# Kernel tuning notes

Measured on AMD Instinct MI355X. Metric: run time of the kernel, lower is better.

Reference implementation:

```python
import jax, jax.numpy as jnp
import numpy as np

N_NODES = 100000
N_EDGES = 1600000
N_GRAPHS = 512
IN_DIM = 128
HID = 128


def setup_inputs() -> dict:
    key = jax.random.key(0)
    ks = jax.random.split(key, 8)
    x = jax.random.normal(ks[0], (N_NODES, IN_DIM), dtype=jnp.float32)
    edge_index = jax.random.randint(ks[1], (2, N_EDGES), 0, N_NODES, dtype=jnp.int64)
    batch = jnp.sort(jax.random.randint(ks[2], (N_NODES,), 0, N_GRAPHS, dtype=jnp.int64))
    s1 = 1.0 / np.sqrt(IN_DIM)
    s2 = 1.0 / np.sqrt(HID)
    W1 = jax.random.normal(ks[3], (IN_DIM, HID), dtype=jnp.float32) * s1
    b1 = jnp.zeros((HID,), dtype=jnp.float32)
    W2 = jax.random.normal(ks[4], (HID, HID), dtype=jnp.float32) * s2
    b2 = jnp.zeros((HID,), dtype=jnp.float32)
    Wp = jax.random.normal(ks[5], (HID, 1), dtype=jnp.float32) * s2
    bp = jnp.zeros((1,), dtype=jnp.float32)
    return {"x": x, "edge_index": edge_index, "batch": batch,
            "W1": W1, "b1": b1, "W2": W2, "b2": b2, "Wp": Wp, "bp": bp}


def _gcn_conv(x, W, b, src, dst, deg_inv_sqrt):
    # PyG GCNConv: linear transform, then normalized scatter-add (self-loops
    # already appended to src/dst), then bias.
    h = x @ W                                   # [N, H]
    norm = deg_inv_sqrt[src] * deg_inv_sqrt[dst]  # [E+N]
    msg = h[src] * norm[:, None]                # gather + scale
    out = jax.ops.segment_sum(msg, dst, num_segments=N_NODES)
    return out + b


def reference(x, edge_index, batch, W1, b1, W2, b2, Wp, bp):
    # Add self-loops once; degree (with self-loops) over target nodes.
    si = jnp.arange(N_NODES, dtype=edge_index.dtype)
    src = jnp.concatenate([edge_index[0], si])
    dst = jnp.concatenate([edge_index[1], si])
    ones = jnp.ones(src.shape[0], dtype=x.dtype)
    deg = jax.ops.segment_sum(ones, dst, num_segments=N_NODES)
    deg_inv_sqrt = jnp.where(deg > 0, jax.lax.rsqrt(jnp.maximum(deg, 1.0)), 0.0)

    h = jax.nn.relu(_gcn_conv(x, W1, b1, src, dst, deg_inv_sqrt))  # dropout = identity (eval)
    h = jax.nn.relu(_gcn_conv(h, W2, b2, src, dst, deg_inv_sqrt))

    # global_mean_pool over graph ids
    sums = jax.ops.segment_sum(h, batch, num_segments=N_GRAPHS)
    cnts = jax.ops.segment_sum(jnp.ones(N_NODES, dtype=h.dtype), batch, num_segments=N_GRAPHS)
    pooled = sums / jnp.maximum(cnts, 1.0)[:, None]               # [G, H]

    return (pooled @ Wp + bp).squeeze(-1)                          # [G]
```

## Files before the change

kernel.cpp:

```cpp
#include <hip/hip_runtime.h>
#include <hip/hip_bf16.h>

#define NN 100000
#define NG 512
#define H  128

typedef _Float16 half8 __attribute__((ext_vector_type(8)));
typedef float f32x4 __attribute__((ext_vector_type(4)));

__global__ __launch_bounds__(256) void k_hist(const int* __restrict__ dst,
                                              int* __restrict__ deg, int E) {
    int e = blockIdx.x * 256 + threadIdx.x;
    if (e < E) atomicAdd(&deg[dst[e]], 1);
}

__global__ __launch_bounds__(256) void k_scan_block(const int* __restrict__ deg,
                                                    int* __restrict__ rowptr,
                                                    int* __restrict__ bsum, int n) {
    __shared__ int s[256];
    int tid = threadIdx.x;
    int i = blockIdx.x * 256 + tid;
    int v = (i < n) ? deg[i] : 0;
    s[tid] = v;
    __syncthreads();
    #pragma unroll
    for (int off = 1; off < 256; off <<= 1) {
        int t = (tid >= off) ? s[tid - off] : 0;
        __syncthreads();
        s[tid] += t;
        __syncthreads();
    }
    if (i < n) rowptr[i] = s[tid] - v;
    if (tid == 255) bsum[blockIdx.x] = s[255];
}

__global__ __launch_bounds__(512) void k_scan_top(int* __restrict__ bsum, int nb) {
    __shared__ int s[512];
    int tid = threadIdx.x;
    int v = (tid < nb) ? bsum[tid] : 0;
    s[tid] = v;
    __syncthreads();
    #pragma unroll
    for (int off = 1; off < 512; off <<= 1) {
        int t = (tid >= off) ? s[tid - off] : 0;
        __syncthreads();
        s[tid] += t;
        __syncthreads();
    }
    if (tid < nb) bsum[tid] = s[tid] - v;
}

__global__ __launch_bounds__(256) void k_scan_fin(int* __restrict__ rowptr,
                                                  const int* __restrict__ bsum,
                                                  const int* __restrict__ deg,
                                                  int* __restrict__ cursor,
                                                  float* __restrict__ dinv,
                                                  int n, int E) {
    int i = blockIdx.x * 256 + threadIdx.x;
    if (i >= n) return;
    int r = rowptr[i] + bsum[i >> 8];
    rowptr[i] = r;
    cursor[i] = r;
    dinv[i] = rsqrtf((float)deg[i] + 1.0f);
    if (i == 0) rowptr[n] = E;
}

__global__ __launch_bounds__(256) void k_wprep(const float* __restrict__ W1,
                                               const float* __restrict__ W2,
                                               _Float16* __restrict__ Wt1,
                                               _Float16* __restrict__ Wt2) {
    int bb = blockIdx.x;
    const float* W = (bb < 64) ? W1 : W2;
    _Float16* Wt = (bb < 64) ? Wt1 : Wt2;
    int i = (bb & 63) * 256 + threadIdx.x;
    int k = i >> 7, n = i & 127;
    Wt[n * 128 + k] = (_Float16)W[i];
}

__global__ __launch_bounds__(256) void k_fill_gemm1(
        const int* __restrict__ src, const int* __restrict__ dst,
        int* __restrict__ cursor, int* __restrict__ col, int E, int nfb,
        const float* __restrict__ x, const _Float16* __restrict__ Wt1,
        const float* __restrict__ dinv, _Float16* __restrict__ tS, int n) {
    if ((int)blockIdx.x < nfb) {
        int e = blockIdx.x * 256 + threadIdx.x;
        if (e >= E) return;
        int d = dst[e];
        int pos = atomicAdd(&cursor[d], 1);
        col[pos] = src[e];
        return;
    }
    const int row0 = ((int)blockIdx.x - nfb) * 64;
    const int tid = threadIdx.x;
    const int w = tid >> 6, lane = tid & 63;
    const int l16 = lane & 15, quad = lane >> 4;
    const int Arow = row0 + w * 16 + l16;
    f32x4 acc[8] = {};
    #pragma unroll
    for (int kk = 0; kk < 4; ++kk) {
        half8 af;
        if (Arow < n) {
            const float* ap = x + (size_t)Arow * H + kk * 32 + quad * 8;
            float4 a0 = ((const float4*)ap)[0];
            float4 a1 = ((const float4*)ap)[1];
            af[0] = (_Float16)a0.x; af[1] = (_Float16)a0.y;
            af[2] = (_Float16)a0.z; af[3] = (_Float16)a0.w;
            af[4] = (_Float16)a1.x; af[5] = (_Float16)a1.y;
            af[6] = (_Float16)a1.z; af[7] = (_Float16)a1.w;
        } else {
            #pragma unroll
            for (int j = 0; j < 8; ++j) af[j] = (_Float16)0.0f;
        }
        #pragma unroll
        for (int nt = 0; nt < 8; ++nt) {
            half8 bf = *((const half8*)(Wt1 + (nt * 16 + l16) * H + kk * 32 + quad * 8));
            acc[nt] = __builtin_amdgcn_mfma_f32_16x16x32_f16(af, bf, acc[nt], 0, 0, 0);
        }
    }
    #pragma unroll
    for (int r = 0; r < 4; ++r) {
        int R = row0 + w * 16 + quad * 4 + r;
        if (R < n) {
            float sc = dinv[R];
            _Float16* crow = tS + (size_t)R * H + l16;
            #pragma unroll
            for (int nt = 0; nt < 8; ++nt)
                crow[nt * 16] = (_Float16)(acc[nt][r] * sc);
        }
    }
}

__global__ __launch_bounds__(256) void k_gemm2(const _Float16* __restrict__ h1,
                                               const _Float16* __restrict__ Wt2,
                                               const float* __restrict__ dinv,
                                               _Float16* __restrict__ tS2, int n) {
    const int row0 = blockIdx.x * 64;
    const int tid = threadIdx.x;
    const int w = tid >> 6, lane = tid & 63;
    const int l16 = lane & 15, quad = lane >> 4;
    const int Arow = row0 + w * 16 + l16;
    f32x4 acc[8] = {};
    #pragma unroll
    for (int kk = 0; kk < 4; ++kk) {
        half8 af;
        if (Arow < n) {
            af = ((const half8*)(h1 + (size_t)Arow * H))[kk * 4 + quad];
        } else {
            #pragma unroll
            for (int j = 0; j < 8; ++j) af[j] = (_Float16)0.0f;
        }
        #pragma unroll
        for (int nt = 0; nt < 8; ++nt) {
            half8 bf = *((const half8*)(Wt2 + (nt * 16 + l16) * H + kk * 32 + quad * 8));
            acc[nt] = __builtin_amdgcn_mfma_f32_16x16x32_f16(af, bf, acc[nt], 0, 0, 0);
        }
    }
    #pragma unroll
    for (int r = 0; r < 4; ++r) {
        int R = row0 + w * 16 + quad * 4 + r;
        if (R < n) {
            float sc = dinv[R];
            _Float16* crow = tS2 + (size_t)R * H + l16;
            #pragma unroll
            for (int nt = 0; nt < 8; ++nt)
                crow[nt * 16] = (_Float16)(acc[nt][r] * sc);
        }
    }
}

__device__ __forceinline__ void gather_rows_h(const half8* __restrict__ t8,
                                              const int* __restrict__ col,
                                              int node, int e0, int end,
                                              float acc[8]) {
    const int lane = threadIdx.x & 63;
    const int q = lane >> 4;
    const int l16 = lane & 15;
    float a0[8] = {}, a1[8] = {};
    if (q == 0) {
        half8 v = t8[(size_t)node * 16 + l16];
        #pragma unroll
        for (int i = 0; i < 8; ++i) a0[i] = (float)v[i];
    }
    for (int base = e0; base < end; base += 64) {
        int ce = base + lane;
        int cidx = (ce < end) ? col[ce] : 0;
        int m = min(64, end - base);
        int nf = m >> 2;
        int g = 0;
        for (; g + 2 <= nf; g += 2) {
            int s0 = __shfl(cidx, 4 * g + q);
            int s1 = __shfl(cidx, 4 * g + 4 + q);
            half8 v0 = t8[(size_t)s0 * 16 + l16];
            half8 v1 = t8[(size_t)s1 * 16 + l16];
            #pragma unroll
            for (int i = 0; i < 8; ++i) {
                a0[i] += (float)v0[i];
                a1[i] += (float)v1[i];
            }
        }
        if (g < nf) {
            int s0 = __shfl(cidx, 4 * g + q);
            half8 v0 = t8[(size_t)s0 * 16 + l16];
            #pragma unroll
            for (int i = 0; i < 8; ++i) a0[i] += (float)v0[i];
        }
        int tail = m & 3;
        if (tail) {
            int s = __shfl(cidx, 4 * nf + q);
            if (q < tail) {
                half8 v = t8[(size_t)s * 16 + l16];
                #pragma unroll
                for (int i = 0; i < 8; ++i) a0[i] += (float)v[i];
            }
        }
    }
    #pragma unroll
    for (int i = 0; i < 8; ++i) {
        float t = a0[i] + a1[i];
        t += __shfl_xor(t, 16);
        t += __shfl_xor(t, 32);
        acc[i] = t;
    }
}

__global__ __launch_bounds__(256) void k_gather1(const _Float16* __restrict__ tS,
                                                 const int* __restrict__ rowptr,
                                                 const int* __restrict__ col,
                                                 const float* __restrict__ dinv,
                                                 const float* __restrict__ b,
                                                 _Float16* __restrict__ out, int n) {
    int node = blockIdx.x * 4 + (threadIdx.x >> 6);
    int lane = threadIdx.x & 63;
    int q = lane >> 4, l16 = lane & 15;
    if (node >= n) return;
    int e0 = rowptr[node], end = rowptr[node + 1];
    float acc[8];
    gather_rows_h((const half8*)tS, col, node, e0, end, acc);
    if (q == 0) {
        float dn = dinv[node];
        const float4* b4 = (const float4*)b;
        float4 bb0 = b4[2 * l16], bb1 = b4[2 * l16 + 1];
        half8 hv;
        hv[0] = (_Float16)fmaxf(dn * acc[0] + bb0.x, 0.0f);
        hv[1] = (_Float16)fmaxf(dn * acc[1] + bb0.y, 0.0f);
        hv[2] = (_Float16)fmaxf(dn * acc[2] + bb0.z, 0.0f);
        hv[3] = (_Float16)fmaxf(dn * acc[3] + bb0.w, 0.0f);
        hv[4] = (_Float16)fmaxf(dn * acc[4] + bb1.x, 0.0f);
        hv[5] = (_Float16)fmaxf(dn * acc[5] + bb1.y, 0.0f);
        hv[6] = (_Float16)fmaxf(dn * acc[6] + bb1.z, 0.0f);
        hv[7] = (_Float16)fmaxf(dn * acc[7] + bb1.w, 0.0f);
        ((half8*)out)[(size_t)node * 16 + l16] = hv;
    }
}

__global__ __launch_bounds__(256) void k_gather2(const _Float16* __restrict__ tS,
                                                 const int* __restrict__ rowptr,
                                                 const int* __restrict__ col,
                                                 const float* __restrict__ dinv,
                                                 const float* __restrict__ b,
                                                 const float* __restrict__ Wp,
                                                 const int* __restrict__ batch,
                                                 float* __restrict__ pool,
                                                 float* __restrict__ cnt, int n) {
    int node = blockIdx.x * 4 + (threadIdx.x >> 6);
    int lane = threadIdx.x & 63;
    int l16 = lane & 15;
    if (node >= n) return;
    int e0 = rowptr[node], end = rowptr[node + 1];
    float acc[8];
    gather_rows_h((const half8*)tS, col, node, e0, end, acc);
    float dn = dinv[node];
    const float4* b4 = (const float4*)b;
    const float4* w4 = (const float4*)Wp;
    float4 bb0 = b4[2 * l16], bb1 = b4[2 * l16 + 1];
    float4 wp0 = w4[2 * l16], wp1 = w4[2 * l16 + 1];
    float s = fmaxf(dn * acc[0] + bb0.x, 0.0f) * wp0.x +
              fmaxf(dn * acc[1] + bb0.y, 0.0f) * wp0.y +
              fmaxf(dn * acc[2] + bb0.z, 0.0f) * wp0.z +
              fmaxf(dn * acc[3] + bb0.w, 0.0f) * wp0.w +
              fmaxf(dn * acc[4] + bb1.x, 0.0f) * wp1.x +
              fmaxf(dn * acc[5] + bb1.y, 0.0f) * wp1.y +
              fmaxf(dn * acc[6] + bb1.z, 0.0f) * wp1.z +
              fmaxf(dn * acc[7] + bb1.w, 0.0f) * wp1.w;
    s += __shfl_xor(s, 1);
    s += __shfl_xor(s, 2);
    s += __shfl_xor(s, 4);
    s += __shfl_xor(s, 8);
    if (lane == 0) {
        int g = batch[node];
        atomicAdd(&pool[g], s);
        atomicAdd(&cnt[g], 1.0f);
    }
}

__global__ __launch_bounds__(256) void final_out_kernel(const float* __restrict__ pool,
                                                        const float* __restrict__ cnt,
                                                        const float* __restrict__ bp,
                                                        float* __restrict__ out, int g) {
    int i = blockIdx.x * 256 + threadIdx.x;
    if (i < g) out[i] = pool[i] / fmaxf(cnt[i], 1.0f) + bp[0];
}

extern "C" void kernel_launch(void* const* d_in, const int* in_sizes, int n_in,
                              void* d_out, int out_size, void* d_ws, size_t ws_size,
                              hipStream_t stream) {
    const float* x     = (const float*)d_in[0];
    const int*   ei    = (const int*)d_in[1];
    const int*   batch = (const int*)d_in[2];
    const float* W1    = (const float*)d_in[3];
    const float* b1    = (const float*)d_in[4];
    const float* W2    = (const float*)d_in[5];
    const float* b2    = (const float*)d_in[6];
    const float* Wp    = (const float*)d_in[7];
    const float* bp    = (const float*)d_in[8];
    float* out = (float*)d_out;

    const int E = in_sizes[1] / 2;
    const int* src = ei;
    const int* dst = ei + E;

    const size_t BUFH = (size_t)NN * H * sizeof(_Float16);
    const size_t NI   = 401408;
    char* ws = (char*)d_ws;
    size_t off = 0;
    _Float16* tS   = (_Float16*)(ws + off); off += BUFH;
    _Float16* h1   = (_Float16*)(ws + off); off += BUFH;
    _Float16* tS2  = (_Float16*)(ws + off); off += BUFH;
    int*      deg  = (int*)     (ws + off); off += NI;
    int*   rowptr  = (int*)     (ws + off); off += NI;
    int*   cursor  = (int*)     (ws + off); off += NI;
    float*    dinv = (float*)   (ws + off); off += NI;
    int*      col  = (int*)     (ws + off); off += ((size_t)E * 4 + 4095) / 4096 * 4096;
    _Float16* Wt1  = (_Float16*)(ws + off); off += 32768;
    _Float16* Wt2  = (_Float16*)(ws + off); off += 32768;
    int*      bsum = (int*)     (ws + off); off += 4096;
    float*    pool = (float*)   (ws + off); off += 2048;
    float*    cnt  = (float*)   (ws + off); off += 2048;

    const int NB  = (NN + 255) / 256;
    const int NFB = (E + 255) / 256;
    const int NGB = (NN + 63) / 64;

    hipMemsetAsync(deg, 0, NN * sizeof(int), stream);
    hipMemsetAsync(pool, 0, 4096, stream);
    k_wprep<<<128, 256, 0, stream>>>(W1, W2, Wt1, Wt2);
    k_hist<<<NFB, 256, 0, stream>>>(dst, deg, E);
    k_scan_block<<<NB, 256, 0, stream>>>(deg, rowptr, bsum, NN);
    k_scan_top<<<1, 512, 0, stream>>>(bsum, NB);
    k_scan_fin<<<NB, 256, 0, stream>>>(rowptr, bsum, deg, cursor, dinv, NN, E);

    k_fill_gemm1<<<NFB + NGB, 256, 0, stream>>>(src, dst, cursor, col, E, NFB,
                                                x, Wt1, dinv, tS, NN);

    k_gather1<<<(NN + 3) / 4, 256, 0, stream>>>(tS, rowptr, col, dinv, b1, h1, NN);
    k_gemm2<<<NGB, 256, 0, stream>>>(h1, Wt2, dinv, tS2, NN);

    k_gather2<<<(NN + 3) / 4, 256, 0, stream>>>(tS2, rowptr, col, dinv, b2, Wp,
                                                batch, pool, cnt, NN);

    final_out_kernel<<<(NG + 255) / 256, 256, 0, stream>>>(pool, cnt, bp, out, NG);
}
```

Before: 688.0 us.

## Split neighbor gathers into feature slices across blocks for cache locality

Replaces the one-wavefront-per-node gather with a feature-sliced scheme. Each block handles one 16-feature slice (32 bytes per row) for 32 nodes, with 8 lanes per node reading half2 values. The intent is to shrink the working set of each gather pass so random row accesses hit in L2/MALL more often, and to raise parallelism per node. The cost is narrower 4-byte loads, repeated reads of the col index for each slice, and pooling partials spread over 8 atomic slots per graph that a final reduction has to sum.

```diff
diff --git a/kernel.cpp b/kernel.cpp
--- a/kernel.cpp
+++ b/kernel.cpp
@@ -6,6 +6,7 @@
 #define H  128
 
 typedef _Float16 half8 __attribute__((ext_vector_type(8)));
+typedef _Float16 half2v __attribute__((ext_vector_type(2)));
 typedef float f32x4 __attribute__((ext_vector_type(4)));
 
 __global__ __launch_bounds__(256) void k_hist(const int* __restrict__ dst,
@@ -168,137 +169,98 @@
     }
 }
 
-__device__ __forceinline__ void gather_rows_h(const half8* __restrict__ t8,
-                                              const int* __restrict__ col,
-                                              int node, int e0, int end,
-                                              float acc[8]) {
+__device__ __forceinline__ float2 gather_slice(const _Float16* __restrict__ tS,
+                                               const int* __restrict__ col,
+                                               int node, int e0, int end, int foff) {
     const int lane = threadIdx.x & 63;
-    const int q = lane >> 4;
-    const int l16 = lane & 15;
-    float a0[8] = {}, a1[8] = {};
-    if (q == 0) {
-        half8 v = t8[(size_t)node * 16 + l16];
+    const int li = lane & 7;
+    const int gb = lane & 56;
+    float ax, ay, bx = 0.f, by = 0.f;
+    {
+        half2v v = *((const half2v*)(tS + (size_t)node * H + foff));
+        ax = (float)v[0]; ay = (float)v[1];
+    }
+    for (int c = e0; c < end; c += 8) {
+        int ce = c + li;
+        int cidx = (ce < end) ? col[ce] : 0;
+        int m = end - c;
         #pragma unroll
-        for (int i = 0; i < 8; ++i) a0[i] = (float)v[i];
-    }
-    for (int base = e0; base < end; base += 64) {
-        int ce = base + lane;
-        int cidx = (ce < end) ? col[ce] : 0;
-        int m = min(64, end - base);
-        int nf = m >> 2;
-        int g = 0;
-        for (; g + 2 <= nf; g += 2) {
-            int s0 = __shfl(cidx, 4 * g + q);
-            int s1 = __shfl(cidx, 4 * g + 4 + q);
-            half8 v0 = t8[(size_t)s0 * 16 + l16];
-            half8 v1 = t8[(size_t)s1 * 16 + l16];
-            #pragma unroll
-            for (int i = 0; i < 8; ++i) {
-                a0[i] += (float)v0[i];
-                a1[i] += (float)v1[i];
-            }
-        }
-        if (g < nf) {
-            int s0 = __shfl(cidx, 4 * g + q);
-            half8 v0 = t8[(size_t)s0 * 16 + l16];
-            #pragma unroll
-            for (int i = 0; i < 8; ++i) a0[i] += (float)v0[i];
-        }
-        int tail = m & 3;
-        if (tail) {
-            int s = __shfl(cidx, 4 * nf + q);
-            if (q < tail) {
-                half8 v = t8[(size_t)s * 16 + l16];
-                #pragma unroll
-                for (int i = 0; i < 8; ++i) a0[i] += (float)v[i];
-            }
-        }
-    }
-    #pragma unroll
-    for (int i = 0; i < 8; ++i) {
-        float t = a0[i] + a1[i];
-        t += __shfl_xor(t, 16);
-        t += __shfl_xor(t, 32);
-        acc[i] = t;
-    }
-}
-
-__global__ __launch_bounds__(256) void k_gather1(const _Float16* __restrict__ tS,
-                                                 const int* __restrict__ rowptr,
-                                                 const int* __restrict__ col,
-                                                 const float* __restrict__ dinv,
-                                                 const float* __restrict__ b,
-                                                 _Float16* __restrict__ out, int n) {
-    int node = blockIdx.x * 4 + (threadIdx.x >> 6);
-    int lane = threadIdx.x & 63;
-    int q = lane >> 4, l16 = lane & 15;
+        for (int j = 0; j < 8; j += 2) {
+            int s0 = __shfl(cidx, gb + j);
+            int s1 = __shfl(cidx, gb + j + 1);
+            half2v v0 = *((const half2v*)(tS + (size_t)s0 * H + foff));
+            half2v v1 = *((const half2v*)(tS + (size_t)s1 * H + foff));
+            bool ok0 = (j < m), ok1 = (j + 1 < m);
+            ax += ok0 ? (float)v0[0] : 0.0f;
+            ay += ok0 ? (float)v0[1] : 0.0f;
+            bx += ok1 ? (float)v1[0] : 0.0f;
+            by += ok1 ? (float)v1[1] : 0.0f;
+        }
+    }
+    return make_float2(ax + bx, ay + by);
+}
+
+__global__ __launch_bounds__(256) void k_gather1s(const _Float16* __restrict__ tS,
+                                                  const int* __restrict__ rowptr,
+                                                  const int* __restrict__ col,
+                                                  const float* __restrict__ dinv,
+                                                  const float* __restrict__ b,
+                                                  _Float16* __restrict__ out, int n) {
+    int f = blockIdx.x & 7;
+    int node = (blockIdx.x >> 3) * 32 + (threadIdx.x >> 3);
     if (node >= n) return;
+    int li = threadIdx.x & 7;
+    int foff = f * 16 + li * 2;
     int e0 = rowptr[node], end = rowptr[node + 1];
-    float acc[8];
-    gather_rows_h((const half8*)tS, col, node, e0, end, acc);
-    if (q == 0) {
-        float dn = dinv[node];
-        const float4* b4 = (const float4*)b;
-        float4 bb0 = b4[2 * l16], bb1 = b4[2 * l16 + 1];
-        half8 hv;
-        hv[0] = (_Float16)fmaxf(dn * acc[0] + bb0.x, 0.0f);
-        hv[1] = (_Float16)fmaxf(dn * acc[1] + bb0.y, 0.0f);
-        hv[2] = (_Float16)fmaxf(dn * acc[2] + bb0.z, 0.0f);
-        hv[3] = (_Float16)fmaxf(dn * acc[3] + bb0.w, 0.0f);
-        hv[4] = (_Float16)fmaxf(dn * acc[4] + bb1.x, 0.0f);
-        hv[5] = (_Float16)fmaxf(dn * acc[5] + bb1.y, 0.0f);
-        hv[6] = (_Float16)fmaxf(dn * acc[6] + bb1.z, 0.0f);
-        hv[7] = (_Float16)fmaxf(dn * acc[7] + bb1.w, 0.0f);
-        ((half8*)out)[(size_t)node * 16 + l16] = hv;
-    }
-}
-
-__global__ __launch_bounds__(256) void k_gather2(const _Float16* __restrict__ tS,
-                                                 const int* __restrict__ rowptr,
-                                                 const int* __restrict__ col,
-                                                 const float* __restrict__ dinv,
-                                                 const float* __restrict__ b,
-                                                 const float* __restrict__ Wp,
-                                                 const int* __restrict__ batch,
-                                                 float* __restrict__ pool,
-                                                 float* __restrict__ cnt, int n) {
-    int node = blockIdx.x * 4 + (threadIdx.x >> 6);
-    int lane = threadIdx.x & 63;
-    int l16 = lane & 15;
+    float2 a = gather_slice(tS, col, node, e0, end, foff);
+    float dn = dinv[node];
+    float2 bb = *((const float2*)(b + foff));
+    half2v hv;
+    hv[0] = (_Float16)fmaxf(dn * a.x + bb.x, 0.0f);
+    hv[1] = (_Float16)fmaxf(dn * a.y + bb.y, 0.0f);
+    *((half2v*)(out + (size_t)node * H + foff)) = hv;
+}
+
+__global__ __launch_bounds__(256) void k_gather2s(const _Float16* __restrict__ tS,
+                                                  const int* __restrict__ rowptr,
+                                                  const int* __restrict__ col,
+                                                  const float* __restrict__ dinv,
+                                                  const float* __restrict__ b,
+                                                  const float* __restrict__ Wp,
+                                                  const int* __restrict__ batch,
+                                                  float* __restrict__ pool8,
+                                                  float* __restrict__ cnt, int n) {
+    int f = blockIdx.x & 7;
+    int node = (blockIdx.x >> 3) * 32 + (threadIdx.x >> 3);
     if (node >= n) return;
+    int li = threadIdx.x & 7;
+    int foff = f * 16 + li * 2;
     int e0 = rowptr[node], end = rowptr[node + 1];
-    float acc[8];
-    gather_rows_h((const half8*)tS, col, node, e0, end, acc);
+    float2 a = gather_slice(tS, col, node, e0, end, foff);
     float dn = dinv[node];
-    const float4* b4 = (const float4*)b;
-    const float4* w4 = (const float4*)Wp;
-    float4 bb0 = b4[2 * l16], bb1 = b4[2 * l16 + 1];
-    float4 wp0 = w4[2 * l16], wp1 = w4[2 * l16 + 1];
-    float s = fmaxf(dn * acc[0] + bb0.x, 0.0f) * wp0.x +
-              fmaxf(dn * acc[1] + bb0.y, 0.0f) * wp0.y +
-              fmaxf(dn * acc[2] + bb0.z, 0.0f) * wp0.z +
-              fmaxf(dn * acc[3] + bb0.w, 0.0f) * wp0.w +
-              fmaxf(dn * acc[4] + bb1.x, 0.0f) * wp1.x +
-              fmaxf(dn * acc[5] + bb1.y, 0.0f) * wp1.y +
-              fmaxf(dn * acc[6] + bb1.z, 0.0f) * wp1.z +
-              fmaxf(dn * acc[7] + bb1.w, 0.0f) * wp1.w;
+    float2 bb = *((const float2*)(b + foff));
+    float2 wp = *((const float2*)(Wp + foff));
+    float s = fmaxf(dn * a.x + bb.x, 0.0f) * wp.x +
+              fmaxf(dn * a.y + bb.y, 0.0f) * wp.y;
     s += __shfl_xor(s, 1);
     s += __shfl_xor(s, 2);
     s += __shfl_xor(s, 4);
-    s += __shfl_xor(s, 8);
-    if (lane == 0) {
+    if (li == 0) {
         int g = batch[node];
-        atomicAdd(&pool[g], s);
-        atomicAdd(&cnt[g], 1.0f);
-    }
-}
-
-__global__ __launch_bounds__(256) void final_out_kernel(const float* __restrict__ pool,
+        atomicAdd(&pool8[g * 8 + f], s);
+        if (f == 0) atomicAdd(&cnt[g], 1.0f);
+    }
+}
+
+__global__ __launch_bounds__(256) void final_out_kernel(const float* __restrict__ pool8,
                                                         const float* __restrict__ cnt,
                                                         const float* __restrict__ bp,
                                                         float* __restrict__ out, int g) {
     int i = blockIdx.x * 256 + threadIdx.x;
-    if (i < g) out[i] = pool[i] / fmaxf(cnt[i], 1.0f) + bp[0];
+    if (i >= g) return;
+    const float* p = pool8 + i * 8;
+    float s = p[0] + p[1] + p[2] + p[3] + p[4] + p[5] + p[6] + p[7];
+    out[i] = s / fmaxf(cnt[i], 1.0f) + bp[0];
 }
 
 extern "C" void kernel_launch(void* const* d_in, const int* in_sizes, int n_in,
@@ -334,15 +296,16 @@
     _Float16* Wt1  = (_Float16*)(ws + off); off += 32768;
     _Float16* Wt2  = (_Float16*)(ws + off); off += 32768;
     int*      bsum = (int*)     (ws + off); off += 4096;
-    float*    pool = (float*)   (ws + off); off += 2048;
+    float*   pool8 = (float*)   (ws + off); off += 16384;
     float*    cnt  = (float*)   (ws + off); off += 2048;
 
     const int NB  = (NN + 255) / 256;
     const int NFB = (E + 255) / 256;
     const int NGB = (NN + 63) / 64;
+    const int NSB = ((NN + 31) / 32) * 8;
 
     hipMemsetAsync(deg, 0, NN * sizeof(int), stream);
-    hipMemsetAsync(pool, 0, 4096, stream);
+    hipMemsetAsync(pool8, 0, 16384 + 2048, stream);
     k_wprep<<<128, 256, 0, stream>>>(W1, W2, Wt1, Wt2);
     k_hist<<<NFB, 256, 0, stream>>>(dst, deg, E);
     k_scan_block<<<NB, 256, 0, stream>>>(deg, rowptr, bsum, NN);
@@ -352,11 +315,11 @@
     k_fill_gemm1<<<NFB + NGB, 256, 0, stream>>>(src, dst, cursor, col, E, NFB,
                                                 x, Wt1, dinv, tS, NN);
 
-    k_gather1<<<(NN + 3) / 4, 256, 0, stream>>>(tS, rowptr, col, dinv, b1, h1, NN);
+    k_gather1s<<<NSB, 256, 0, stream>>>(tS, rowptr, col, dinv, b1, h1, NN);
     k_gemm2<<<NGB, 256, 0, stream>>>(h1, Wt2, dinv, tS2, NN);
 
-    k_gather2<<<(NN + 3) / 4, 256, 0, stream>>>(tS2, rowptr, col, dinv, b2, Wp,
-                                                batch, pool, cnt, NN);
-
-    final_out_kernel<<<(NG + 255) / 256, 256, 0, stream>>>(pool, cnt, bp, out, NG);
-}
+    k_gather2s<<<NSB, 256, 0, stream>>>(tS2, rowptr, col, dinv, b2, Wp,
+                                        batch, pool8, cnt, NN);
+
+    final_out_kernel<<<(NG + 255) / 256, 256, 0, stream>>>(pool8, cnt, bp, out, NG);
+}
```

New measurement: 1.452 ms. 2.11x slower.
